# Optimization experiments

Hardware: AMD Instinct MI355X
Metric: run time of the kernel (lower is better)

## Reference

```python
import jax, jax.numpy as jnp
import numpy as np
from jax import lax

K = 3        # KBA kernel size
GC = 4       # channels per group numerator (gc in torch code): g = c // GC
EPS = 1e-6   # LayerNorm2d eps


def conv2d(x, w, b=None, pad=0, groups=1):
    out = lax.conv_general_dilated(x, w, (1, 1), [(pad, pad), (pad, pad)],
                                   dimension_numbers=('NCHW', 'OIHW', 'NCHW'),
                                   feature_group_count=groups)
    return out if b is None else out + b[None, :, None, None]


def layernorm2d(x, w, b):
    mu = jnp.mean(x, axis=1, keepdims=True)
    var = jnp.mean((x - mu) ** 2, axis=1, keepdims=True)
    y = (x - mu) / jnp.sqrt(var + EPS)
    return w[None, :, None, None] * y + b[None, :, None, None]


def kba_fn(x, att, selfb, selfw):
    # x: (B,c,H,W) features; att: (B,nset,H,W) mixing coeffs
    B, c, H, W = x.shape
    nset = att.shape[1]
    g = c // GC; cg = GC; KK = K * K
    a = att.reshape(B, nset, H * W).transpose(0, 2, 1)              # (B,HW,nset)
    bias = a @ selfb[0]                                             # (B,HW,c)
    attk = (a @ selfw[0]).reshape(B, H * W, g, cg, cg * KK)         # per-pixel kernels
    pad = K // 2
    xp = jnp.pad(x, ((0, 0), (0, 0), (pad, pad), (pad, pad)))
    # im2col / unfold, channel-major then kernel position (matches torch unfold)
    patches = jnp.stack([xp[:, :, i:i + H, j:j + W] for i in range(K) for j in range(K)], axis=2)  # (B,c,KK,H,W)
    uf = patches.reshape(B, g, cg * KK, H * W).transpose(0, 3, 1, 2)  # (B,HW,g,cg*KK)
    out = jnp.einsum('bpgij,bpgj->bpgi', attk, uf).reshape(B, H * W, c) + bias
    return out.transpose(0, 2, 1).reshape(B, c, H, W)


def petformer(x, n1w, n1b, n2w, n2b,
              kdw1, kdw2, kc1a, kc1b, kproj,
              c2a_w, c2a_b, c2b_w, c2b_b, c211_w, c211_b,
              kw, kb, attgamma, ga1,
              temp, qkv_w, qkv_dw_w, mproj_w,
              ca1_w, ca1_b, ca2_w, ca2_b):
    B, C, H, W = x.shape
    # channel attention: global avg pool + 1x1 conv
    gap = jnp.mean(x, axis=(2, 3), keepdims=True)
    ca1 = conv2d(gap, ca1_w, ca1_b)
    ca2 = conv2d(gap, ca2_w, ca2_b)

    # ---- KBA branch ----
    xn = layernorm2d(x, n1w, n1b)
    hid = kdw1.shape[0]
    x1 = conv2d(conv2d(xn, kdw1), kdw2, pad=1, groups=hid)          # dwconv path
    interc = c2a_w.shape[0]
    a = conv2d(xn, c2a_w, c2a_b, pad=1, groups=interc)              # grouped 3x3
    a1, a2 = jnp.split(a, 2, axis=1)                                # SimpleGate
    a = conv2d(a1 * a2, c2b_w, c2b_b)                               # 1x1 -> nset
    att = a * attgamma + conv2d(xn, c211_w, c211_b)
    uf = conv2d(conv2d(xn, kc1a), kc1b, pad=1, groups=hid)          # conv1 path
    x2 = kba_fn(uf, att, kb, kw) * ga1 + uf
    kba_out = conv2d(jax.nn.gelu(x1, approximate=False) * x2, kproj)

    # ---- MDTA branch (transposed channel attention) ----
    xm = layernorm2d(x, n2w, n2b)
    qkv = conv2d(conv2d(xm, qkv_w), qkv_dw_w, pad=1, groups=3 * C)
    q, k, v = jnp.split(qkv, 3, axis=1)
    heads = temp.shape[0]
    _h = lambda t: t.reshape(B, heads, C // heads, H * W)
    q, k, v = _h(q), _h(k), _h(v)
    q = q / jnp.maximum(jnp.linalg.norm(q, axis=-1, keepdims=True), 1e-12)
    k = k / jnp.maximum(jnp.linalg.norm(k, axis=-1, keepdims=True), 1e-12)
    attn = jax.nn.softmax(jnp.einsum('bhcp,bhdp->bhcd', q, k) * temp, axis=-1)
    out = jnp.einsum('bhcd,bhdp->bhcp', attn, v).reshape(B, C, H, W)
    mdta_out = conv2d(out, mproj_w)

    return x + kba_out * ca1 + mdta_out * ca2


def setup_inputs() -> dict:
    key = jax.random.key(0)
    ks = iter(jax.random.split(key, 40))
    nrm = lambda shape, s=0.1: (jax.random.normal(next(ks), shape) * s).astype(jnp.float32)
    B, C, H, W = 4, 48, 64, 64
    HID, NSET, HEADS, INTERC = 96, 32, 8, 24
    return {
        'x': jax.random.normal(next(ks), (B, C, H, W), jnp.float32),
        'n1w': jnp.ones((C,), jnp.float32), 'n1b': jnp.zeros((C,), jnp.float32),
        'n2w': jnp.ones((C,), jnp.float32), 'n2b': jnp.zeros((C,), jnp.float32),
        'kdw1': nrm((HID, C, 1, 1)), 'kdw2': nrm((HID, 1, 3, 3)),
        'kc1a': nrm((HID, C, 1, 1)), 'kc1b': nrm((HID, 1, 3, 3)),
        'kproj': nrm((C, HID, 1, 1)),
        'c2a_w': nrm((INTERC, C // INTERC, 3, 3)), 'c2a_b': jnp.zeros((INTERC,), jnp.float32),
        'c2b_w': nrm((NSET, INTERC // 2, 1, 1)), 'c2b_b': jnp.zeros((NSET,), jnp.float32),
        'c211_w': nrm((NSET, C, 1, 1)), 'c211_b': jnp.zeros((NSET,), jnp.float32),
        'kw': nrm((1, NSET, HID * GC * K * K), 0.02), 'kb': nrm((1, NSET, HID), 0.02),
        'attgamma': jnp.full((1, NSET, 1, 1), 0.01, jnp.float32),
        'ga1': jnp.full((1, HID, 1, 1), 0.01, jnp.float32),
        'temp': jnp.ones((HEADS, 1, 1), jnp.float32),
        'qkv_w': nrm((3 * C, C, 1, 1)), 'qkv_dw_w': nrm((3 * C, 1, 3, 3)),
        'mproj_w': nrm((C, C, 1, 1)),
        'ca1_w': nrm((C, C, 1, 1)), 'ca1_b': jnp.zeros((C,), jnp.float32),
        'ca2_w': nrm((C, C, 1, 1)), 'ca2_b': jnp.zeros((C,), jnp.float32),
    }


def reference(x, n1w, n1b, n2w, n2b,
              kdw1, kdw2, kc1a, kc1b, kproj,
              c2a_w, c2a_b, c2b_w, c2b_b, c211_w, c211_b,
              kw, kb, attgamma, ga1,
              temp, qkv_w, qkv_dw_w, mproj_w,
              ca1_w, ca1_b, ca2_w, ca2_b):
    return petformer(x, n1w, n1b, n2w, n2b, kdw1, kdw2, kc1a, kc1b, kproj,
                     c2a_w, c2a_b, c2b_w, c2b_b, c211_w, c211_b,
                     kw, kb, attgamma, ga1, temp, qkv_w, qkv_dw_w, mproj_w,
                     ca1_w, ca1_b, ca2_w, ca2_b)
```

## Files before the change

kernel.cpp:

```cpp
#include <hip/hip_runtime.h>
#include <hip/hip_bf16.h>
#include <cstdint>

typedef unsigned short ushortT;
typedef __attribute__((ext_vector_type(8))) short short8;
typedef __attribute__((ext_vector_type(4))) float f32x4;

static constexpr int Bn = 4, Cc = 48, Hh = 64, Wd = 64, HW = 4096;
static constexpr int HID = 96, NSET = 32, INTERC = 24, HEADS = 8, CPH = 6;

static constexpr int FXN   = 0;
static constexpr int FA    = 786432;
static constexpr int FB    = 2359296;
static constexpr int FC    = 3932160;
static constexpr int FD    = 5505024;
static constexpr int FARAW = 7077888;
static constexpr int FATT  = 7471104;
static constexpr int FGAP  = 8781824;
static constexpr int FSP   = 8782400;
static constexpr int FW    = 8790000;
static constexpr int FATTB = 8937200;
static constexpr int FWT   = 9199344;
static constexpr int FXNB  = 9260784;
static constexpr int FXMB  = 9785072;
static constexpr int FHBF  = 10309360;
static constexpr int FWPW  = 11095792;
static constexpr int FWQK  = 11102960;
static constexpr int FWKP  = 11107568;
static constexpr int FWMP  = 11109872;
static constexpr int FQKVR = 11111424;

static constexpr int W_N1W=0, W_N1B=48, W_N2W=96, W_N2B=144;
static constexpr int W_KDW1=192, W_KDW2=4800, W_KC1A=5664, W_KC1B=10272;
static constexpr int W_KPROJ=11136, W_C2AW=15744, W_C2AB=16176;
static constexpr int W_C2BW=16200, W_C2BB=16584, W_C211W=16616, W_C211B=18152;
static constexpr int W_KW=18184, W_KB=128776, W_ATTG=131848, W_GA1=131880;
static constexpr int W_TEMP=131976, W_QKVW=131984, W_QKVDW=138896, W_MPROJ=140192;
static constexpr int W_CA1W=142496, W_CA1B=144800, W_CA2W=144848, W_CA2B=147152;

__device__ __forceinline__ float b2f(ushortT u) {
    union { uint32_t i; float f; } v; v.i = ((uint32_t)u) << 16; return v.f;
}
__device__ __forceinline__ ushortT f2b(float f) {
    union { float f; uint32_t i; } v; v.f = f;
    uint32_t i = v.i;
    uint32_t lsb = (i >> 16) & 1u;
    i += 0x7fffu + lsb;
    return (ushortT)(i >> 16);
}
__device__ __forceinline__ int dtype_bf16(const uint32_t* n1w_raw) {
    return n1w_raw[0] == 0x3F803F80u;
}
__device__ __forceinline__ ushortT raw_bf(const void* p, int idx, int fl) {
    return fl ? ((const ushortT*)p)[idx] : f2b(((const float*)p)[idx]);
}
__device__ __forceinline__ float raw_f(const void* p, int idx, int fl) {
    return fl ? b2f(((const ushortT*)p)[idx]) : ((const float*)p)[idx];
}

struct ConvPack {
    const void* src[27];
    int dstoff[27];
    int n[27];
};
struct RawW {
    const void* kdw1; const void* kc1a; const void* c211w; const void* qkvw;
    const void* kproj; const void* mproj; const void* kw; const void* kb;
    const void* n1w; const void* n1b; const void* n2w; const void* n2b;
};

__global__ void k_prep(ConvPack p, RawW rw, float* __restrict__ dst,
                       ushortT* __restrict__ Wt, ushortT* __restrict__ Wpw,
                       ushortT* __restrict__ Wqk, ushortT* __restrict__ Wkp,
                       ushortT* __restrict__ Wmp,
                       const void* __restrict__ x, float* __restrict__ gap,
                       float* __restrict__ xn, ushortT* __restrict__ xnb,
                       ushortT* __restrict__ xmb,
                       const uint32_t* __restrict__ n1w_raw) {
    int fl = dtype_bf16(n1w_raw);
    int y = blockIdx.y;
    if (y < 27) {
        int n = p.n[y];
        for (int i = blockIdx.x * 256 + threadIdx.x; i < n; i += 64 * 256) {
            dst[p.dstoff[y] + i] = raw_f(p.src[y], i, fl);
        }
    } else if (y == 27) {
        for (int u = blockIdx.x * 256 + threadIdx.x; u < 24 * 160 * 32; u += 64 * 256) {
            int n = u & 31;
            int rest = u >> 5;
            int r = rest % 160;
            int gr = rest / 160;
            ushortT out;
            if (r < 144) {
                int j = r >> 2, i = r & 3;
                out = raw_bf(rw.kw, n * 3456 + gr * 144 + i * 36 + j, fl);
            } else if (r < 148) {
                out = raw_bf(rw.kb, n * HID + gr * 4 + (r - 144), fl);
            } else out = 0;
            Wt[u] = out;
        }
    } else if (y == 28) {
        for (int u = blockIdx.x * 256 + threadIdx.x; u < 224 * 64; u += 64 * 256) {
            int co = u >> 6, c = u & 63;
            ushortT v = 0;
            if (c < 48) {
                if (co < 96)       v = raw_bf(rw.kdw1,  co * 48 + c, fl);
                else if (co < 192) v = raw_bf(rw.kc1a,  (co - 96) * 48 + c, fl);
                else               v = raw_bf(rw.c211w, (co - 192) * 48 + c, fl);
            }
            Wpw[u] = v;
        }
    } else if (y == 29) {
        for (int u = blockIdx.x * 256 + threadIdx.x; u < 144 * 64; u += 64 * 256) {
            int co = u >> 6, c = u & 63;
            Wqk[u] = (c < 48) ? raw_bf(rw.qkvw, co * 48 + c, fl) : (ushortT)0;
        }
    } else if (y == 30) {
        for (int u = blockIdx.x * 256 + threadIdx.x; u < 48 * 96; u += 64 * 256) {
            int co = u / 96, c = u % 96;
            Wkp[u] = raw_bf(rw.kproj, co * 96 + c, fl);
        }
    } else if (y == 31) {
        for (int u = blockIdx.x * 256 + threadIdx.x; u < 48 * 64; u += 64 * 256) {
            int co = u >> 6, c = u & 63;
            Wmp[u] = (c < 48) ? raw_bf(rw.mproj, co * 48 + c, fl) : (ushortT)0;
        }
    } else if (y == 32) {
        __shared__ float red[4];
        for (int bc = blockIdx.x; bc < Bn * Cc; bc += 64) {
            float s = 0.f;
            if (fl) {
                const ushortT* xb = (const ushortT*)x + bc * HW;
                for (int i = threadIdx.x; i < HW; i += 256) s += b2f(xb[i]);
            } else {
                const float* xb = (const float*)x + bc * HW;
                for (int i = threadIdx.x; i < HW; i += 256) s += xb[i];
            }
            #pragma unroll
            for (int o = 32; o > 0; o >>= 1) s += __shfl_down(s, o);
            int lane = threadIdx.x & 63, wv = threadIdx.x >> 6;
            if (lane == 0) red[wv] = s;
            __syncthreads();
            if (threadIdx.x == 0)
                gap[bc] = (red[0] + red[1] + red[2] + red[3]) * (1.f / HW);
            __syncthreads();
        }
    } else {
        int pp = blockIdx.x * 256 + threadIdx.x;
        int b = pp >> 12, hw = pp & 4095;
        float xr[Cc];
        if (fl) {
            const ushortT* xb = (const ushortT*)x + b * Cc * HW + hw;
            #pragma unroll
            for (int c = 0; c < Cc; c++) xr[c] = b2f(xb[c * HW]);
        } else {
            const float* xb = (const float*)x + b * Cc * HW + hw;
            #pragma unroll
            for (int c = 0; c < Cc; c++) xr[c] = xb[c * HW];
        }
        float s = 0.f, ss = 0.f;
        #pragma unroll
        for (int c = 0; c < Cc; c++) { s += xr[c]; ss += xr[c] * xr[c]; }
        float mu = s * (1.f / Cc);
        float var = ss * (1.f / Cc) - mu * mu;
        float r = rsqrtf(var + 1e-6f);
        uint32_t pn[32], pm[32];
        #pragma unroll
        for (int i = 0; i < 24; i++) {
            float y0 = (xr[2 * i] - mu) * r, y1 = (xr[2 * i + 1] - mu) * r;
            float n0 = raw_f(rw.n1w, 2 * i, fl) * y0 + raw_f(rw.n1b, 2 * i, fl);
            float n1 = raw_f(rw.n1w, 2 * i + 1, fl) * y1 + raw_f(rw.n1b, 2 * i + 1, fl);
            float m0 = raw_f(rw.n2w, 2 * i, fl) * y0 + raw_f(rw.n2b, 2 * i, fl);
            float m1 = raw_f(rw.n2w, 2 * i + 1, fl) * y1 + raw_f(rw.n2b, 2 * i + 1, fl);
            xn[(b * Cc + 2 * i) * HW + hw] = n0;
            xn[(b * Cc + 2 * i + 1) * HW + hw] = n1;
            pn[i] = (uint32_t)f2b(n0) | ((uint32_t)f2b(n1) << 16);
            pm[i] = (uint32_t)f2b(m0) | ((uint32_t)f2b(m1) << 16);
        }
        #pragma unroll
        for (int i = 24; i < 32; i++) { pn[i] = 0; pm[i] = 0; }
        uint4* dn = (uint4*)(xnb + (size_t)pp * 64);
        uint4* dm = (uint4*)(xmb + (size_t)pp * 64);
        #pragma unroll
        for (int qd = 0; qd < 8; qd++) {
            uint4 v; v.x = pn[qd*4]; v.y = pn[qd*4+1]; v.z = pn[qd*4+2]; v.w = pn[qd*4+3];
            dn[qd] = v;
            uint4 u; u.x = pm[qd*4]; u.y = pm[qd*4+1]; u.z = pm[qd*4+2]; u.w = pm[qd*4+3];
            dm[qd] = u;
        }
    }
}

__global__ void __launch_bounds__(256) k_pw1m(const ushortT* __restrict__ xnb, const ushortT* __restrict__ xmb,
                       const ushortT* __restrict__ Wpw, const ushortT* __restrict__ Wqk,
                       const float* __restrict__ wts, float* __restrict__ t1,
                       float* __restrict__ t2, float* __restrict__ attn_t,
                       float* __restrict__ qkvr) {
    int wave = threadIdx.x >> 6, lane = threadIdx.x & 63;
    int m = lane & 15, q = lane >> 4;
    int p = blockIdx.x * 64 + wave * 16 + m;
    int b = p >> 12, hw = p & 4095;
    short8 B0 = *(const short8*)(xnb + (size_t)p * 64 + q * 8);
    short8 B1 = *(const short8*)(xnb + (size_t)p * 64 + 32 + q * 8);
    #pragma unroll
    for (int t = 0; t < 14; t++) {
        short8 A0 = *(const short8*)(Wpw + (16 * t + m) * 64 + q * 8);
        short8 A1 = *(const short8*)(Wpw + (16 * t + m) * 64 + 32 + q * 8);
        f32x4 z = {0.f, 0.f, 0.f, 0.f};
        f32x4 D = __builtin_amdgcn_mfma_f32_16x16x32_bf16(A0, B0, z, 0, 0, 0);
        D = __builtin_amdgcn_mfma_f32_16x16x32_bf16(A1, B1, D, 0, 0, 0);
        #pragma unroll
        for (int g = 0; g < 4; g++) {
            int co = 16 * t + 4 * q + g;
            if (t < 6) t1[(b * HID + co) * HW + hw] = D[g];
            else if (t < 12) t2[(b * HID + (co - 96)) * HW + hw] = D[g];
            else {
                int n = co - 192;
                attn_t[(size_t)p * 32 + n] = D[g] + wts[W_C211B + n];
            }
        }
    }
    short8 C0 = *(const short8*)(xmb + (size_t)p * 64 + q * 8);
    short8 C1 = *(const short8*)(xmb + (size_t)p * 64 + 32 + q * 8);
    #pragma unroll
    for (int t = 0; t < 9; t++) {
        short8 A0 = *(const short8*)(Wqk + (16 * t + m) * 64 + q * 8);
        short8 A1 = *(const short8*)(Wqk + (16 * t + m) * 64 + 32 + q * 8);
        f32x4 z = {0.f, 0.f, 0.f, 0.f};
        f32x4 D = __builtin_amdgcn_mfma_f32_16x16x32_bf16(A0, C0, z, 0, 0, 0);
        D = __builtin_amdgcn_mfma_f32_16x16x32_bf16(A1, C1, D, 0, 0, 0);
        #pragma unroll
        for (int g = 0; g < 4; g++) {
            int co = 16 * t + 4 * q + g;
            qkvr[(b * 144 + co) * HW + hw] = D[g];
        }
    }
}

__global__ void __launch_bounds__(256) k_dw(const float* __restrict__ t1, const float* __restrict__ t2,
                     const float* __restrict__ xn, const float* __restrict__ wts,
                     float* __restrict__ x1g, float* __restrict__ uf, float* __restrict__ araw) {
    int y = blockIdx.y;
    int pbase = blockIdx.x * 1024 + threadIdx.x * 4;
    int b = pbase >> 12, hw = pbase & 4095, h = hw >> 6, w0 = hw & 63;

    if (y < 192) {
        int c = (y < 96) ? y : y - 96;
        const float* base = (y < 96) ? t1 : t2;
        const float* wk = wts + ((y < 96) ? W_KDW2 : W_KC1B) + c * 9;
        const float* plane = base + (b * HID + c) * HW;

        float a0 = 0.f, a1 = 0.f, a2 = 0.f, a3 = 0.f;
        #pragma unroll
        for (int ki = 0; ki < 3; ki++) {
            int hh = h + ki - 1;
            if ((unsigned)hh < 64u) {
                const float* row = plane + hh * 64 + w0;
                float4 mm = *(const float4*)row;
                float lf = (w0 > 0) ? row[-1] : 0.f;
                float rt = (w0 < 60) ? row[4] : 0.f;
                float k0 = wk[ki * 3], k1 = wk[ki * 3 + 1], k2 = wk[ki * 3 + 2];
                a0 += k0 * lf   + k1 * mm.x + k2 * mm.y;
                a1 += k0 * mm.x + k1 * mm.y + k2 * mm.z;
                a2 += k0 * mm.y + k1 * mm.z + k2 * mm.w;
                a3 += k0 * mm.z + k1 * mm.w + k2 * rt;
            }
        }
        int idx = (b * HID + c) * HW + hw;
        if (y < 96) {
            float4 g;
            g.x = 0.5f * a0 * (1.f + erff(a0 * 0.70710678118654752f));
            g.y = 0.5f * a1 * (1.f + erff(a1 * 0.70710678118654752f));
            g.z = 0.5f * a2 * (1.f + erff(a2 * 0.70710678118654752f));
            g.w = 0.5f * a3 * (1.f + erff(a3 * 0.70710678118654752f));
            *(float4*)(x1g + idx) = g;
        } else {
            float4 o; o.x = a0; o.y = a1; o.z = a2; o.w = a3;
            *(float4*)(uf + idx) = o;
        }
    } else {
        int o = y - 192;
        float bias = wts[W_C2AB + o];
        float a0 = bias, a1 = bias, a2 = bias, a3 = bias;
        #pragma unroll
        for (int ic = 0; ic < 2; ic++) {
            const float* plane = xn + (b * Cc + 2 * o + ic) * HW;
            const float* wk = wts + W_C2AW + (o * 2 + ic) * 9;
            #pragma unroll
            for (int ki = 0; ki < 3; ki++) {
                int hh = h + ki - 1;
                if ((unsigned)hh < 64u) {
                    const float* row = plane + hh * 64 + w0;
                    float4 mm = *(const float4*)row;
                    float lf = (w0 > 0) ? row[-1] : 0.f;
                    float rt = (w0 < 60) ? row[4] : 0.f;
                    float k0 = wk[ki * 3], k1 = wk[ki * 3 + 1], k2 = wk[ki * 3 + 2];
                    a0 += k0 * lf   + k1 * mm.x + k2 * mm.y;
                    a1 += k0 * mm.x + k1 * mm.y + k2 * mm.z;
                    a2 += k0 * mm.y + k1 * mm.z + k2 * mm.w;
                    a3 += k0 * mm.z + k1 * mm.w + k2 * rt;
                }
            }
        }
        float4 out; out.x = a0; out.y = a1; out.z = a2; out.w = a3;
        *(float4*)(araw + (b * INTERC + o) * HW + hw) = out;
    }
}

__global__ void __launch_bounds__(256) k_attq(const float* __restrict__ qkvr, const float* __restrict__ araw,
                      const float* __restrict__ attn_t, const float* __restrict__ wts,
                      float* __restrict__ qkv, ushortT* __restrict__ att_bf) {
    int y = blockIdx.y;
    if (y < 144) {
        int ch = y;
        const float* wk = wts + W_QKVDW + ch * 9;
        int pbase = blockIdx.x * 1024 + threadIdx.x * 4;
        int b = pbase >> 12, hw = pbase & 4095, h = hw >> 6, w0 = hw & 63;
        const float* plane = qkvr + (b * 144 + ch) * HW;

        float a0 = 0.f, a1 = 0.f, a2 = 0.f, a3 = 0.f;
        #pragma unroll
        for (int ki = 0; ki < 3; ki++) {
            int hh = h + ki - 1;
            if ((unsigned)hh < 64u) {
                const float* row = plane + hh * 64 + w0;
                float4 mm = *(const float4*)row;
                float lf = (w0 > 0) ? row[-1] : 0.f;
                float rt = (w0 < 60) ? row[4] : 0.f;
                float k0 = wk[ki * 3], k1 = wk[ki * 3 + 1], k2 = wk[ki * 3 + 2];
                a0 += k0 * lf   + k1 * mm.x + k2 * mm.y;
                a1 += k0 * mm.x + k1 * mm.y + k2 * mm.z;
                a2 += k0 * mm.y + k1 * mm.z + k2 * mm.w;
                a3 += k0 * mm.z + k1 * mm.w + k2 * rt;
            }
        }
        float4 o; o.x = a0; o.y = a1; o.z = a2; o.w = a3;
        *(float4*)(qkv + (b * 144 + ch) * HW + hw) = o;
    } else {
        int p = ((y - 144) * 16 + blockIdx.x) * 256 + threadIdx.x;
        int b = p >> 12, hw = p & 4095;
        const float* ab = araw + b * INTERC * HW + hw;
        float sg[12];
        #pragma unroll
        for (int i = 0; i < 12; i++) sg[i] = ab[i * HW] * ab[(12 + i) * HW];
        const float* ct = attn_t + (size_t)p * 32;
        uint32_t packed[16];
        #pragma unroll
        for (int nq = 0; nq < 16; nq++) {
            float v2[2];
            #pragma unroll
            for (int u = 0; u < 2; u++) {
                int n = nq * 2 + u;
                float a = wts[W_C2BB + n];
                #pragma unroll
                for (int c = 0; c < 12; c++) a += wts[W_C2BW + n * 12 + c] * sg[c];
                v2[u] = wts[W_ATTG + n] * a + ct[n];
            }
            packed[nq] = (uint32_t)f2b(v2[0]) | ((uint32_t)f2b(v2[1]) << 16);
        }
        uint4* dst = (uint4*)(att_bf + (size_t)p * 32);
        #pragma unroll
        for (int qd = 0; qd < 4; qd++) {
            uint4 v; v.x = packed[qd*4]; v.y = packed[qd*4+1]; v.z = packed[qd*4+2]; v.w = packed[qd*4+3];
            dst[qd] = v;
        }
    }
}

__global__ void __launch_bounds__(256) k_kbas(const ushortT* __restrict__ att_bf, const float* __restrict__ uf,
                     const float* __restrict__ x1g, const ushortT* __restrict__ Wt,
                     const float* __restrict__ wts, ushortT* __restrict__ h_bf,
                     const float* __restrict__ qkv, float* __restrict__ Sp) {
    if (blockIdx.y < 24) {
        int wave = threadIdx.x >> 6, lane = threadIdx.x & 63;
        int m = lane & 15, q = lane >> 4;
        int gr = blockIdx.y;

        short8 A[10];
        const ushortT* wtg = Wt + gr * 160 * 32;
        #pragma unroll
        for (int t = 0; t < 10; t++)
            A[t] = *(const short8*)(wtg + (16 * t + m) * 32 + q * 8);

        for (int tile = 0; tile < 4; tile++) {
            int p = blockIdx.x * 256 + wave * 64 + tile * 16 + m;
            int b = p >> 12, hw = p & 4095, h = hw >> 6, w = hw & 63;

            short8 Bf = *(const short8*)(att_bf + (size_t)p * 32 + q * 8);

            f32x4 D[10];
            #pragma unroll
            for (int t = 0; t < 10; t++) {
                f32x4 z = {0.f, 0.f, 0.f, 0.f};
                D[t] = __builtin_amdgcn_mfma_f32_16x16x32_bf16(A[t], Bf, z, 0, 0, 0);
            }

            float s0 = 0.f, s1 = 0.f, s2 = 0.f, s3 = 0.f;
            #pragma unroll
            for (int t = 0; t < 9; t++) {
                int j = 4 * t + q;
                int ci = j / 9;
                int kk = j - 9 * ci;
                int ki = kk / 3, kj = kk - 3 * ki;
                int hh = h + ki - 1, ww = w + kj - 1;
                float tap = 0.f;
                if ((unsigned)hh < 64u && (unsigned)ww < 64u)
                    tap = uf[(b * HID + gr * 4 + ci) * HW + hh * 64 + ww];
                s0 += D[t][0] * tap;
                s1 += D[t][1] * tap;
                s2 += D[t][2] * tap;
                s3 += D[t][3] * tap;
            }
            s0 += D[9][0]; s1 += D[9][1]; s2 += D[9][2]; s3 += D[9][3];

            s0 += __shfl_xor(s0, 16); s0 += __shfl_xor(s0, 32);
            s1 += __shfl_xor(s1, 16); s1 += __shfl_xor(s1, 32);
            s2 += __shfl_xor(s2, 16); s2 += __shfl_xor(s2, 32);
            s3 += __shfl_xor(s3, 16); s3 += __shfl_xor(s3, 32);

            float sel = (q == 0) ? s0 : ((q == 1) ? s1 : ((q == 2) ? s2 : s3));
            int ch = gr * 4 + q;
            int idx = (b * HID + ch) * HW + hw;
            float x2 = sel * wts[W_GA1 + ch] + uf[idx];
            float hv = x1g[idx] * x2;
            h_bf[(size_t)p * 96 + ch] = f2b(hv);
        }
    } else {
        int sub = (blockIdx.y - 24) * 64 + blockIdx.x;
        int bh = sub & 31, chunk = sub >> 5;
        int b = bh / HEADS, hd = bh % HEADS;
        const float* qb = qkv + (b * 144 + hd * CPH) * HW;
        const float* kb = qkv + (b * 144 + 48 + hd * CPH) * HW;
        float acc[48];
        #pragma unroll
        for (int t = 0; t < 48; t++) acc[t] = 0.f;
        #pragma unroll
        for (int i = 0; i < 4; i++) {
            int px = chunk * 1024 + i * 256 + threadIdx.x;
            float qv[CPH], kv[CPH];
            #pragma unroll
            for (int c = 0; c < CPH; c++) { qv[c] = qb[c * HW + px]; kv[c] = kb[c * HW + px]; }
            #pragma unroll
            for (int c = 0; c < CPH; c++) {
                #pragma unroll
                for (int d = 0; d < CPH; d++) acc[c * CPH + d] += qv[c] * kv[d];
                acc[36 + c] += qv[c] * qv[c];
                acc[42 + c] += kv[c] * kv[c];
            }
        }
        __shared__ float red[48 * 4];
        int lane = threadIdx.x & 63, wv = threadIdx.x >> 6;
        #pragma unroll
        for (int t = 0; t < 48; t++) {
            float v = acc[t];
            #pragma unroll
            for (int o = 32; o > 0; o >>= 1) v += __shfl_down(v, o);
            if (lane == 0) red[t * 4 + wv] = v;
        }
        __syncthreads();
        if (threadIdx.x < 48)
            Sp[(bh * 4 + chunk) * 48 + threadIdx.x] =
                red[threadIdx.x * 4] + red[threadIdx.x * 4 + 1] +
                red[threadIdx.x * 4 + 2] + red[threadIdx.x * 4 + 3];
    }
}

__global__ void __launch_bounds__(256) k_finalm(const void* __restrict__ x, const uint32_t* __restrict__ n1w_raw,
                        const ushortT* __restrict__ h_bf, const ushortT* __restrict__ Wkp,
                        const ushortT* __restrict__ Wmp, const float* __restrict__ qkv,
                        const float* __restrict__ Sp, const float* __restrict__ gap,
                        const float* __restrict__ wts, void* __restrict__ out) {
    int fl = dtype_bf16(n1w_raw);
    int wave = threadIdx.x >> 6, lane = threadIdx.x & 63;
    int m = lane & 15, q = lane >> 4;
    int p = blockIdx.x * 64 + wave * 16 + m;
    int hw = p & 4095;
    int bblk = (blockIdx.x * 64) >> 12;

    __shared__ float sm[384];
    __shared__ float S_l[288];
    __shared__ float caL[96];
    for (int i = threadIdx.x; i < 384; i += 256) {
        int hd = i / 48, k = i % 48;
        int bh = bblk * HEADS + hd;
        sm[i] = Sp[(bh * 4 + 0) * 48 + k] + Sp[(bh * 4 + 1) * 48 + k]
              + Sp[(bh * 4 + 2) * 48 + k] + Sp[(bh * 4 + 3) * 48 + k];
    }
    __syncthreads();
    if (threadIdx.x < 48) {
        int hd = threadIdx.x / 6, c = threadIdx.x % 6;
        const float* base = sm + hd * 48;
        float rqv = 1.f / fmaxf(sqrtf(base[36 + c]), 1e-12f);
        float tmp = wts[W_TEMP + hd];
        float row[CPH];
        #pragma unroll
        for (int d = 0; d < CPH; d++) {
            float rkv = 1.f / fmaxf(sqrtf(base[42 + d]), 1e-12f);
            row[d] = base[c * CPH + d] * rqv * rkv * tmp;
        }
        float mx = row[0];
        #pragma unroll
        for (int d = 1; d < CPH; d++) mx = fmaxf(mx, row[d]);
        float sum = 0.f;
        #pragma unroll
        for (int d = 0; d < CPH; d++) { row[d] = expf(row[d] - mx); sum += row[d]; }
        float inv = 1.f / sum;
        #pragma unroll
        for (int d = 0; d < CPH; d++) S_l[hd * 36 + c * CPH + d] = row[d] * inv;
    }
    if (threadIdx.x >= 64 && threadIdx.x < 160) {
        int i = threadIdx.x - 64;
        int which = i / 48, co = i % 48;
        const float* g = gap + bblk * Cc;
        float sacc = wts[(which ? W_CA2B : W_CA1B) + co];
        #pragma unroll
        for (int c = 0; c < Cc; c++)
            sacc += wts[(which ? W_CA2W : W_CA1W) + co * Cc + c] * g[c];
        caL[i] = sacc;
    }
    __syncthreads();

    short8 H0 = *(const short8*)(h_bf + (size_t)p * 96 + q * 8);
    short8 H1 = *(const short8*)(h_bf + (size_t)p * 96 + 32 + q * 8);
    short8 H2 = *(const short8*)(h_bf + (size_t)p * 96 + 64 + q * 8);
    f32x4 Dk[3];
    #pragma unroll
    for (int t = 0; t < 3; t++) {
        short8 A0 = *(const short8*)(Wkp + (16 * t + m) * 96 + q * 8);
        short8 A1 = *(const short8*)(Wkp + (16 * t + m) * 96 + 32 + q * 8);
        short8 A2 = *(const short8*)(Wkp + (16 * t + m) * 96 + 64 + q * 8);
        f32x4 z = {0.f, 0.f, 0.f, 0.f};
        f32x4 D = __builtin_amdgcn_mfma_f32_16x16x32_bf16(A0, H0, z, 0, 0, 0);
        D = __builtin_amdgcn_mfma_f32_16x16x32_bf16(A1, H1, D, 0, 0, 0);
        Dk[t] = __builtin_amdgcn_mfma_f32_16x16x32_bf16(A2, H2, D, 0, 0, 0);
    }

    const float* vbase = qkv + (bblk * 144 + 96) * HW + hw;
    short8 Bm0, Bm1;
    #pragma unroll
    for (int jj = 0; jj < 8; jj++) {
        int c0 = q * 8 + jj;
        int hd0 = c0 / 6, cc0 = c0 - 6 * hd0;
        float a = 0.f;
        #pragma unroll
        for (int d = 0; d < CPH; d++)
            a += S_l[hd0 * 36 + cc0 * 6 + d] * vbase[(hd0 * 6 + d) * HW];
        Bm0[jj] = (short)f2b(a);
        int c1 = 32 + q * 8 + jj;
        float bv = 0.f;
        if (c1 < 48) {
            int hd1 = c1 / 6, cc1 = c1 - 6 * hd1;
            #pragma unroll
            for (int d = 0; d < CPH; d++)
                bv += S_l[hd1 * 36 + cc1 * 6 + d] * vbase[(hd1 * 6 + d) * HW];
        }
        Bm1[jj] = (short)f2b(bv);
    }

    #pragma unroll
    for (int t = 0; t < 3; t++) {
        short8 A0 = *(const short8*)(Wmp + (16 * t + m) * 64 + q * 8);
        short8 A1 = *(const short8*)(Wmp + (16 * t + m) * 64 + 32 + q * 8);
        f32x4 z = {0.f, 0.f, 0.f, 0.f};
        f32x4 D = __builtin_amdgcn_mfma_f32_16x16x32_bf16(A0, Bm0, z, 0, 0, 0);
        D = __builtin_amdgcn_mfma_f32_16x16x32_bf16(A1, Bm1, D, 0, 0, 0);
        #pragma unroll
        for (int g = 0; g < 4; g++) {
            int co = 16 * t + 4 * q + g;
            int idx = (bblk * Cc + co) * HW + hw;
            float xv = fl ? b2f(((const ushortT*)x)[idx]) : ((const float*)x)[idx];
            float res = xv + Dk[t][g] * caL[co] + D[g] * caL[48 + co];
            if (fl) ((ushortT*)out)[idx] = f2b(res);
            else    ((float*)out)[idx] = res;
        }
    }
}

extern "C" void kernel_launch(void* const* d_in, const int* in_sizes, int n_in,
                              void* d_out, int out_size, void* d_ws, size_t ws_size,
                              hipStream_t stream) {
    float* ws_f = (float*)d_ws;

    float* xn    = ws_f + FXN;
    float* bufA  = ws_f + FA;
    float* bufB  = ws_f + FB;
    float* bufC  = ws_f + FC;
    float* bufD  = ws_f + FD;
    float* araw  = ws_f + FARAW;
    float* attn_t= ws_f + FATT;
    float* gap   = ws_f + FGAP;
    float* Sp    = ws_f + FSP;
    float* wts   = ws_f + FW;
    ushortT* att_bf  = (ushortT*)(ws_f + FATTB);
    ushortT* Wt      = (ushortT*)(ws_f + FWT);
    ushortT* xnb     = (ushortT*)(ws_f + FXNB);
    ushortT* xmb     = (ushortT*)(ws_f + FXMB);
    ushortT* h_bf    = (ushortT*)(ws_f + FHBF);
    ushortT* Wpw     = (ushortT*)(ws_f + FWPW);
    ushortT* Wqk     = (ushortT*)(ws_f + FWQK);
    ushortT* Wkp     = (ushortT*)(ws_f + FWKP);
    ushortT* Wmp     = (ushortT*)(ws_f + FWMP);
    float* qkvr      = ws_f + FQKVR;

    float* qkv  = bufC;
    const uint32_t* n1w_raw = (const uint32_t*)d_in[1];

    static const int wsizes[27] = {48,48,48,48,4608,864,4608,864,4608,432,24,384,32,
                                   1536,32,110592,3072,32,96,8,6912,1296,2304,2304,48,2304,48};
    static const int woffs[27] = {W_N1W,W_N1B,W_N2W,W_N2B,W_KDW1,W_KDW2,W_KC1A,W_KC1B,
                                  W_KPROJ,W_C2AW,W_C2AB,W_C2BW,W_C2BB,W_C211W,W_C211B,
                                  W_KW,W_KB,W_ATTG,W_GA1,W_TEMP,W_QKVW,W_QKVDW,W_MPROJ,
                                  W_CA1W,W_CA1B,W_CA2W,W_CA2B};
    ConvPack cp;
    for (int i = 0; i < 27; i++) {
        cp.src[i] = d_in[i + 1];
        cp.dstoff[i] = woffs[i];
        cp.n[i] = wsizes[i];
    }
    RawW rw;
    rw.kdw1 = d_in[5]; rw.kc1a = d_in[7]; rw.c211w = d_in[14]; rw.qkvw = d_in[21];
    rw.kproj = d_in[9]; rw.mproj = d_in[23]; rw.kw = d_in[16]; rw.kb = d_in[17];
    rw.n1w = d_in[1]; rw.n1b = d_in[2]; rw.n2w = d_in[3]; rw.n2b = d_in[4];

    k_prep<<<dim3(64, 34), 256, 0, stream>>>(cp, rw, wts, Wt, Wpw, Wqk, Wkp, Wmp,
                                             d_in[0], gap, xn, xnb, xmb, n1w_raw);
    k_pw1m<<<dim3(256), 256, 0, stream>>>(xnb, xmb, Wpw, Wqk, wts, bufA, bufB, attn_t, qkvr);
    k_dw<<<dim3(16, 216), 256, 0, stream>>>(bufA, bufB, xn, wts, bufC, bufD, araw);
    k_attq<<<dim3(16, 148), 256, 0, stream>>>(qkvr, araw, attn_t, wts, qkv, att_bf);
    k_kbas<<<dim3(64, 26), 256, 0, stream>>>(att_bf, bufD, bufC, Wt, wts, h_bf, qkv, Sp);
    k_finalm<<<dim3(256), 256, 0, stream>>>(d_in[0], n1w_raw, h_bf, Wkp, Wmp,
                                            qkv, Sp, gap, wts, d_out);
}
```

Before: 222.1 us.

## Rebalance kernel stages: split pw1m grid, merge qkv dwconv into k_dw, regroup attention

k_pw1m now splits its two GEMM halves across a second grid dimension, so each block does either the pointwise-projection GEMM or the qkv GEMM, doubling parallelism. The qkv depthwise conv moves from k_attq into k_dw, which widens that grid to 360 rows, and qkv gets its own workspace buffer instead of aliasing bufC. The attention softmax/packing and the Gram partial sums now share a new kernel, k_attsm, and the KBA MFMA kernel stands alone. The intent is to cut the serial dependency depth and fill the GPU better. The cost is an extra workspace region and a different block-count balance per kernel.

Result: no change. 221.9 us (-0.1%).

```diff
diff --git a/kernel.cpp b/kernel.cpp
--- a/kernel.cpp
+++ b/kernel.cpp
@@ -29,6 +29,7 @@
 static constexpr int FWKP  = 11107568;
 static constexpr int FWMP  = 11109872;
 static constexpr int FQKVR = 11111424;
+static constexpr int FQKV  = 13470720;
 
 static constexpr int W_N1W=0, W_N1B=48, W_N2W=96, W_N2B=144;
 static constexpr int W_KDW1=192, W_KDW2=4800, W_KC1A=5664, W_KC1B=10272;
@@ -200,46 +201,51 @@
     int m = lane & 15, q = lane >> 4;
     int p = blockIdx.x * 64 + wave * 16 + m;
     int b = p >> 12, hw = p & 4095;
-    short8 B0 = *(const short8*)(xnb + (size_t)p * 64 + q * 8);
-    short8 B1 = *(const short8*)(xnb + (size_t)p * 64 + 32 + q * 8);
-    #pragma unroll
-    for (int t = 0; t < 14; t++) {
-        short8 A0 = *(const short8*)(Wpw + (16 * t + m) * 64 + q * 8);
-        short8 A1 = *(const short8*)(Wpw + (16 * t + m) * 64 + 32 + q * 8);
-        f32x4 z = {0.f, 0.f, 0.f, 0.f};
-        f32x4 D = __builtin_amdgcn_mfma_f32_16x16x32_bf16(A0, B0, z, 0, 0, 0);
-        D = __builtin_amdgcn_mfma_f32_16x16x32_bf16(A1, B1, D, 0, 0, 0);
-        #pragma unroll
-        for (int g = 0; g < 4; g++) {
-            int co = 16 * t + 4 * q + g;
-            if (t < 6) t1[(b * HID + co) * HW + hw] = D[g];
-            else if (t < 12) t2[(b * HID + (co - 96)) * HW + hw] = D[g];
-            else {
-                int n = co - 192;
-                attn_t[(size_t)p * 32 + n] = D[g] + wts[W_C211B + n];
-            }
-        }
-    }
-    short8 C0 = *(const short8*)(xmb + (size_t)p * 64 + q * 8);
-    short8 C1 = *(const short8*)(xmb + (size_t)p * 64 + 32 + q * 8);
-    #pragma unroll
-    for (int t = 0; t < 9; t++) {
-        short8 A0 = *(const short8*)(Wqk + (16 * t + m) * 64 + q * 8);
-        short8 A1 = *(const short8*)(Wqk + (16 * t + m) * 64 + 32 + q * 8);
-        f32x4 z = {0.f, 0.f, 0.f, 0.f};
-        f32x4 D = __builtin_amdgcn_mfma_f32_16x16x32_bf16(A0, C0, z, 0, 0, 0);
-        D = __builtin_amdgcn_mfma_f32_16x16x32_bf16(A1, C1, D, 0, 0, 0);
-        #pragma unroll
-        for (int g = 0; g < 4; g++) {
-            int co = 16 * t + 4 * q + g;
-            qkvr[(b * 144 + co) * HW + hw] = D[g];
+    if (blockIdx.y == 0) {
+        short8 B0 = *(const short8*)(xnb + (size_t)p * 64 + q * 8);
+        short8 B1 = *(const short8*)(xnb + (size_t)p * 64 + 32 + q * 8);
+        #pragma unroll
+        for (int t = 0; t < 14; t++) {
+            short8 A0 = *(const short8*)(Wpw + (16 * t + m) * 64 + q * 8);
+            short8 A1 = *(const short8*)(Wpw + (16 * t + m) * 64 + 32 + q * 8);
+            f32x4 z = {0.f, 0.f, 0.f, 0.f};
+            f32x4 D = __builtin_amdgcn_mfma_f32_16x16x32_bf16(A0, B0, z, 0, 0, 0);
+            D = __builtin_amdgcn_mfma_f32_16x16x32_bf16(A1, B1, D, 0, 0, 0);
+            #pragma unroll
+            for (int g = 0; g < 4; g++) {
+                int co = 16 * t + 4 * q + g;
+                if (t < 6) t1[(b * HID + co) * HW + hw] = D[g];
+                else if (t < 12) t2[(b * HID + (co - 96)) * HW + hw] = D[g];
+                else {
+                    int n = co - 192;
+                    attn_t[(size_t)p * 32 + n] = D[g] + wts[W_C211B + n];
+                }
+            }
+        }
+    } else {
+        short8 C0 = *(const short8*)(xmb + (size_t)p * 64 + q * 8);
+        short8 C1 = *(const short8*)(xmb + (size_t)p * 64 + 32 + q * 8);
+        #pragma unroll
+        for (int t = 0; t < 9; t++) {
+            short8 A0 = *(const short8*)(Wqk + (16 * t + m) * 64 + q * 8);
+            short8 A1 = *(const short8*)(Wqk + (16 * t + m) * 64 + 32 + q * 8);
+            f32x4 z = {0.f, 0.f, 0.f, 0.f};
+            f32x4 D = __builtin_amdgcn_mfma_f32_16x16x32_bf16(A0, C0, z, 0, 0, 0);
+            D = __builtin_amdgcn_mfma_f32_16x16x32_bf16(A1, C1, D, 0, 0, 0);
+            #pragma unroll
+            for (int g = 0; g < 4; g++) {
+                int co = 16 * t + 4 * q + g;
+                qkvr[(b * 144 + co) * HW + hw] = D[g];
+            }
         }
     }
 }
 
 __global__ void __launch_bounds__(256) k_dw(const float* __restrict__ t1, const float* __restrict__ t2,
-                     const float* __restrict__ xn, const float* __restrict__ wts,
-                     float* __restrict__ x1g, float* __restrict__ uf, float* __restrict__ araw) {
+                     const float* __restrict__ xn, const float* __restrict__ qkvr,
+                     const float* __restrict__ wts,
+                     float* __restrict__ x1g, float* __restrict__ uf,
+                     float* __restrict__ araw, float* __restrict__ qkv) {
     int y = blockIdx.y;
     int pbase = blockIdx.x * 1024 + threadIdx.x * 4;
     int b = pbase >> 12, hw = pbase & 4095, h = hw >> 6, w0 = hw & 63;
@@ -278,7 +284,7 @@
             float4 o; o.x = a0; o.y = a1; o.z = a2; o.w = a3;
             *(float4*)(uf + idx) = o;
         }
-    } else {
+    } else if (y < 216) {
         int o = y - 192;
         float bias = wts[W_C2AB + o];
         float a0 = bias, a1 = bias, a2 = bias, a3 = bias;
@@ -304,18 +310,9 @@
         }
         float4 out; out.x = a0; out.y = a1; out.z = a2; out.w = a3;
         *(float4*)(araw + (b * INTERC + o) * HW + hw) = out;
-    }
-}
-
-__global__ void __launch_bounds__(256) k_attq(const float* __restrict__ qkvr, const float* __restrict__ araw,
-                      const float* __restrict__ attn_t, const float* __restrict__ wts,
-                      float* __restrict__ qkv, ushortT* __restrict__ att_bf) {
-    int y = blockIdx.y;
-    if (y < 144) {
-        int ch = y;
+    } else {
+        int ch = y - 216;
         const float* wk = wts + W_QKVDW + ch * 9;
-        int pbase = blockIdx.x * 1024 + threadIdx.x * 4;
-        int b = pbase >> 12, hw = pbase & 4095, h = hw >> 6, w0 = hw & 63;
         const float* plane = qkvr + (b * 144 + ch) * HW;
 
         float a0 = 0.f, a1 = 0.f, a2 = 0.f, a3 = 0.f;
@@ -336,8 +333,14 @@
         }
         float4 o; o.x = a0; o.y = a1; o.z = a2; o.w = a3;
         *(float4*)(qkv + (b * 144 + ch) * HW + hw) = o;
-    } else {
-        int p = ((y - 144) * 16 + blockIdx.x) * 256 + threadIdx.x;
+    }
+}
+
+__global__ void __launch_bounds__(256) k_attsm(const float* __restrict__ araw, const float* __restrict__ attn_t,
+                       const float* __restrict__ qkv, const float* __restrict__ wts,
+                       ushortT* __restrict__ att_bf, float* __restrict__ Sp) {
+    if (blockIdx.x < 64) {
+        int p = blockIdx.x * 256 + threadIdx.x;
         int b = p >> 12, hw = p & 4095;
         const float* ab = araw + b * INTERC * HW + hw;
         float sg[12];
@@ -364,69 +367,8 @@
             uint4 v; v.x = packed[qd*4]; v.y = packed[qd*4+1]; v.z = packed[qd*4+2]; v.w = packed[qd*4+3];
             dst[qd] = v;
         }
-    }
-}
-
-__global__ void __launch_bounds__(256) k_kbas(const ushortT* __restrict__ att_bf, const float* __restrict__ uf,
-                     const float* __restrict__ x1g, const ushortT* __restrict__ Wt,
-                     const float* __restrict__ wts, ushortT* __restrict__ h_bf,
-                     const float* __restrict__ qkv, float* __restrict__ Sp) {
-    if (blockIdx.y < 24) {
-        int wave = threadIdx.x >> 6, lane = threadIdx.x & 63;
-        int m = lane & 15, q = lane >> 4;
-        int gr = blockIdx.y;
-
-        short8 A[10];
-        const ushortT* wtg = Wt + gr * 160 * 32;
-        #pragma unroll
-        for (int t = 0; t < 10; t++)
-            A[t] = *(const short8*)(wtg + (16 * t + m) * 32 + q * 8);
-
-        for (int tile = 0; tile < 4; tile++) {
-            int p = blockIdx.x * 256 + wave * 64 + tile * 16 + m;
-            int b = p >> 12, hw = p & 4095, h = hw >> 6, w = hw & 63;
-
-            short8 Bf = *(const short8*)(att_bf + (size_t)p * 32 + q * 8);
-
-            f32x4 D[10];
-            #pragma unroll
-            for (int t = 0; t < 10; t++) {
-                f32x4 z = {0.f, 0.f, 0.f, 0.f};
-                D[t] = __builtin_amdgcn_mfma_f32_16x16x32_bf16(A[t], Bf, z, 0, 0, 0);
-            }
-
-            float s0 = 0.f, s1 = 0.f, s2 = 0.f, s3 = 0.f;
-            #pragma unroll
-            for (int t = 0; t < 9; t++) {
-                int j = 4 * t + q;
-                int ci = j / 9;
-                int kk = j - 9 * ci;
-                int ki = kk / 3, kj = kk - 3 * ki;
-                int hh = h + ki - 1, ww = w + kj - 1;
-                float tap = 0.f;
-                if ((unsigned)hh < 64u && (unsigned)ww < 64u)
-                    tap = uf[(b * HID + gr * 4 + ci) * HW + hh * 64 + ww];
-                s0 += D[t][0] * tap;
-                s1 += D[t][1] * tap;
-                s2 += D[t][2] * tap;
-                s3 += D[t][3] * tap;
-            }
-            s0 += D[9][0]; s1 += D[9][1]; s2 += D[9][2]; s3 += D[9][3];
-
-            s0 += __shfl_xor(s0, 16); s0 += __shfl_xor(s0, 32);
-            s1 += __shfl_xor(s1, 16); s1 += __shfl_xor(s1, 32);
-            s2 += __shfl_xor(s2, 16); s2 += __shfl_xor(s2, 32);
-            s3 += __shfl_xor(s3, 16); s3 += __shfl_xor(s3, 32);
-
-            float sel = (q == 0) ? s0 : ((q == 1) ? s1 : ((q == 2) ? s2 : s3));
-            int ch = gr * 4 + q;
-            int idx = (b * HID + ch) * HW + hw;
-            float x2 = sel * wts[W_GA1 + ch] + uf[idx];
-            float hv = x1g[idx] * x2;
-            h_bf[(size_t)p * 96 + ch] = f2b(hv);
-        }
     } else {
-        int sub = (blockIdx.y - 24) * 64 + blockIdx.x;
+        int sub = blockIdx.x - 64;
         int bh = sub & 31, chunk = sub >> 5;
         int b = bh / HEADS, hd = bh % HEADS;
         const float* qb = qkv + (b * 144 + hd * CPH) * HW;
@@ -462,6 +404,64 @@
             Sp[(bh * 4 + chunk) * 48 + threadIdx.x] =
                 red[threadIdx.x * 4] + red[threadIdx.x * 4 + 1] +
                 red[threadIdx.x * 4 + 2] + red[threadIdx.x * 4 + 3];
+    }
+}
+
+__global__ void __launch_bounds__(256) k_kba(const ushortT* __restrict__ att_bf, const float* __restrict__ uf,
+                     const float* __restrict__ x1g, const ushortT* __restrict__ Wt,
+                     const float* __restrict__ wts, ushortT* __restrict__ h_bf) {
+    int wave = threadIdx.x >> 6, lane = threadIdx.x & 63;
+    int m = lane & 15, q = lane >> 4;
+    int gr = blockIdx.y;
+
+    short8 A[10];
+    const ushortT* wtg = Wt + gr * 160 * 32;
+    #pragma unroll
+    for (int t = 0; t < 10; t++)
+        A[t] = *(const short8*)(wtg + (16 * t + m) * 32 + q * 8);
+
+    for (int tile = 0; tile < 4; tile++) {
+        int p = blockIdx.x * 256 + wave * 64 + tile * 16 + m;
+        int b = p >> 12, hw = p & 4095, h = hw >> 6, w = hw & 63;
+
+        short8 Bf = *(const short8*)(att_bf + (size_t)p * 32 + q * 8);
+
+        f32x4 D[10];
+        #pragma unroll
+        for (int t = 0; t < 10; t++) {
+            f32x4 z = {0.f, 0.f, 0.f, 0.f};
+            D[t] = __builtin_amdgcn_mfma_f32_16x16x32_bf16(A[t], Bf, z, 0, 0, 0);
+        }
+
+        float s0 = 0.f, s1 = 0.f, s2 = 0.f, s3 = 0.f;
+        #pragma unroll
+        for (int t = 0; t < 9; t++) {
+            int j = 4 * t + q;
+            int ci = j / 9;
+            int kk = j - 9 * ci;
+            int ki = kk / 3, kj = kk - 3 * ki;
+            int hh = h + ki - 1, ww = w + kj - 1;
+            float tap = 0.f;
+            if ((unsigned)hh < 64u && (unsigned)ww < 64u)
+                tap = uf[(b * HID + gr * 4 + ci) * HW + hh * 64 + ww];
+            s0 += D[t][0] * tap;
+            s1 += D[t][1] * tap;
+            s2 += D[t][2] * tap;
+            s3 += D[t][3] * tap;
+        }
+        s0 += D[9][0]; s1 += D[9][1]; s2 += D[9][2]; s3 += D[9][3];
+
+        s0 += __shfl_xor(s0, 16); s0 += __shfl_xor(s0, 32);
+        s1 += __shfl_xor(s1, 16); s1 += __shfl_xor(s1, 32);
+        s2 += __shfl_xor(s2, 16); s2 += __shfl_xor(s2, 32);
+        s3 += __shfl_xor(s3, 16); s3 += __shfl_xor(s3, 32);
+
+        float sel = (q == 0) ? s0 : ((q == 1) ? s1 : ((q == 2) ? s2 : s3));
+        int ch = gr * 4 + q;
+        int idx = (b * HID + ch) * HW + hw;
+        float x2 = sel * wts[W_GA1 + ch] + uf[idx];
+        float hv = x1g[idx] * x2;
+        h_bf[(size_t)p * 96 + ch] = f2b(hv);
     }
 }
 
@@ -584,8 +584,8 @@
     float* xn    = ws_f + FXN;
     float* bufA  = ws_f + FA;
     float* bufB  = ws_f + FB;
-    float* bufC  = ws_f + FC;
-    float* bufD  = ws_f + FD;
+    float* x1g   = ws_f + FC;
+    float* uf    = ws_f + FD;
     float* araw  = ws_f + FARAW;
     float* attn_t= ws_f + FATT;
     float* gap   = ws_f + FGAP;
@@ -601,8 +601,8 @@
     ushortT* Wkp     = (ushortT*)(ws_f + FWKP);
     ushortT* Wmp     = (ushortT*)(ws_f + FWMP);
     float* qkvr      = ws_f + FQKVR;
-
-    float* qkv  = bufC;
+    float* qkv       = ws_f + FQKV;
+
     const uint32_t* n1w_raw = (const uint32_t*)d_in[1];
 
     static const int wsizes[27] = {48,48,48,48,4608,864,4608,864,4608,432,24,384,32,
@@ -624,10 +624,10 @@
 
     k_prep<<<dim3(64, 34), 256, 0, stream>>>(cp, rw, wts, Wt, Wpw, Wqk, Wkp, Wmp,
                                              d_in[0], gap, xn, xnb, xmb, n1w_raw);
-    k_pw1m<<<dim3(256), 256, 0, stream>>>(xnb, xmb, Wpw, Wqk, wts, bufA, bufB, attn_t, qkvr);
-    k_dw<<<dim3(16, 216), 256, 0, stream>>>(bufA, bufB, xn, wts, bufC, bufD, araw);
-    k_attq<<<dim3(16, 148), 256, 0, stream>>>(qkvr, araw, attn_t, wts, qkv, att_bf);
-    k_kbas<<<dim3(64, 26), 256, 0, stream>>>(att_bf, bufD, bufC, Wt, wts, h_bf, qkv, Sp);
+    k_pw1m<<<dim3(256, 2), 256, 0, stream>>>(xnb, xmb, Wpw, Wqk, wts, bufA, bufB, attn_t, qkvr);
+    k_dw<<<dim3(16, 360), 256, 0, stream>>>(bufA, bufB, xn, qkvr, wts, x1g, uf, araw, qkv);
+    k_attsm<<<dim3(192), 256, 0, stream>>>(araw, attn_t, qkv, wts, att_bf, Sp);
+    k_kba<<<dim3(64, 24), 256, 0, stream>>>(att_bf, uf, x1g, Wt, wts, h_bf);
     k_finalm<<<dim3(256), 256, 0, stream>>>(d_in[0], n1w_raw, h_bf, Wkp, Wmp,
                                             qkv, Sp, gap, wts, d_out);
 }
```
